# Kernel optimization log

Hardware: AMD Instinct MI355X
Metric: run time of the kernel (lower is better)

The kernel has to match this reference:

```python
import jax, jax.numpy as jnp
import numpy as np

SEQ, IN, H = 64, 100000, 50


def setup_inputs() -> dict:
    key = jax.random.key(0)
    k0, k1, k2, k3, k4 = jax.random.split(key, 5)
    x = jax.random.normal(k0, (SEQ, 1, IN), dtype=jnp.float32) * 0.02
    Wi = jax.random.normal(k1, (IN, 4 * H), dtype=jnp.float32) * 0.01
    bi = jax.random.normal(k2, (4 * H,), dtype=jnp.float32) * 0.01
    Wh = jax.random.normal(k3, (H, 4 * H), dtype=jnp.float32) * 0.1
    bh = jax.random.normal(k4, (4 * H,), dtype=jnp.float32) * 0.01
    return {"x": x, "Wi": Wi, "bi": bi, "Wh": Wh, "bh": bh}


def reference(x, Wi, bi, Wh, bh):
    # x: [seq, batch=1, input_size] -- each row is a flattened ParameterList.
    # Precompute the input projection for all steps at once (one big GEMM),
    # same math as per-step input_weights(input) since it has no recurrence.
    gates_in = jnp.einsum('sbi,ig->sbg', x, Wi) + bi + bh  # [seq, 1, 4H]

    def step(carry, g_in):
        hx, cx = carry
        gates = g_in + hx @ Wh  # [1, 4H]
        i, f, g, o = jnp.split(gates, 4, axis=1)
        i = jax.nn.sigmoid(i)
        f = jax.nn.sigmoid(f)
        g = jnp.tanh(g)
        o = jax.nn.sigmoid(o)
        cy = f * cx + i * g
        hy = o * jnp.tanh(cy)
        return (hy, cy), None

    h0 = jnp.zeros((1, H), dtype=x.dtype)
    c0 = jnp.zeros((1, H), dtype=x.dtype)
    (h_final, _), _ = jax.lax.scan(step, (h0, c0), gates_in)
    # torch.squeeze(out_hidden): (1, H) -> (H,)
    return jnp.squeeze(h_final)
```

## Files before the change

### kernel.cpp

```cpp
#include <hip/hip_runtime.h>
#include <hip/hip_bf16.h>


#define K_DIM 100000
#define NG 200
#define NS 64
#define TK 32
#define NBLK 512
#define KSTRIDE (NBLK * TK)
#define CELLS (NS * NG)
#define XS_STRIDE 68

__global__ __launch_bounds__(512, 4) void k1_gemm_partial(
    const float* __restrict__ x, const float* __restrict__ Wi,
    float* __restrict__ partial)
{
    __shared__ float4 ws4[TK * 50];
    __shared__ float  xs[TK * XS_STRIDE];

    const int tid  = threadIdx.x;
    const int lane = tid & 63;
    const int wave = tid >> 6;
    const int s0   = wave * 8;

    const int sx = tid >> 3;
    const int kq = (tid & 7) << 2;
    const float4* wi4 = (const float4*)Wi;

    float4 acc4[8];
#pragma unroll
    for (int j = 0; j < 8; ++j) acc4[j] = make_float4(0.f, 0.f, 0.f, 0.f);

    int kt = blockIdx.x * TK;

    float4 w0, w1, w2, w3 = make_float4(0.f, 0.f, 0.f, 0.f), xr;
    {
        const float4* wt = wi4 + (size_t)kt * 50;
        w0 = wt[tid];
        w1 = wt[tid + 512];
        w2 = wt[tid + 1024];
        if (tid < 64) w3 = wt[tid + 1536];
        xr = *(const float4*)(x + (size_t)sx * K_DIM + kt + kq);
    }

    for (; kt < K_DIM; kt += KSTRIDE) {
        __syncthreads();
        ws4[tid]        = w0;
        ws4[tid + 512]  = w1;
        ws4[tid + 1024] = w2;
        if (tid < 64) ws4[tid + 1536] = w3;
        xs[(kq + 0) * XS_STRIDE + sx] = xr.x;
        xs[(kq + 1) * XS_STRIDE + sx] = xr.y;
        xs[(kq + 2) * XS_STRIDE + sx] = xr.z;
        xs[(kq + 3) * XS_STRIDE + sx] = xr.w;
        __syncthreads();

        int ktn = kt + KSTRIDE;
        if (ktn < K_DIM) {
            const float4* wt = wi4 + (size_t)ktn * 50;
            w0 = wt[tid];
            w1 = wt[tid + 512];
            w2 = wt[tid + 1024];
            if (tid < 64) w3 = wt[tid + 1536];
            xr = *(const float4*)(x + (size_t)sx * K_DIM + ktn + kq);
        }

        if (lane < 50) {
#pragma unroll 4
            for (int k = 0; k < TK; ++k) {
                float4 wv = ws4[k * 50 + lane];
                const float4* xrow = (const float4*)(xs + k * XS_STRIDE + s0);
                float4 xa = xrow[0];
                float4 xb = xrow[1];
                acc4[0].x = fmaf(wv.x, xa.x, acc4[0].x);
                acc4[0].y = fmaf(wv.y, xa.x, acc4[0].y);
                acc4[0].z = fmaf(wv.z, xa.x, acc4[0].z);
                acc4[0].w = fmaf(wv.w, xa.x, acc4[0].w);
                acc4[1].x = fmaf(wv.x, xa.y, acc4[1].x);
                acc4[1].y = fmaf(wv.y, xa.y, acc4[1].y);
                acc4[1].z = fmaf(wv.z, xa.y, acc4[1].z);
                acc4[1].w = fmaf(wv.w, xa.y, acc4[1].w);
                acc4[2].x = fmaf(wv.x, xa.z, acc4[2].x);
                acc4[2].y = fmaf(wv.y, xa.z, acc4[2].y);
                acc4[2].z = fmaf(wv.z, xa.z, acc4[2].z);
                acc4[2].w = fmaf(wv.w, xa.z, acc4[2].w);
                acc4[3].x = fmaf(wv.x, xa.w, acc4[3].x);
                acc4[3].y = fmaf(wv.y, xa.w, acc4[3].y);
                acc4[3].z = fmaf(wv.z, xa.w, acc4[3].z);
                acc4[3].w = fmaf(wv.w, xa.w, acc4[3].w);
                acc4[4].x = fmaf(wv.x, xb.x, acc4[4].x);
                acc4[4].y = fmaf(wv.y, xb.x, acc4[4].y);
                acc4[4].z = fmaf(wv.z, xb.x, acc4[4].z);
                acc4[4].w = fmaf(wv.w, xb.x, acc4[4].w);
                acc4[5].x = fmaf(wv.x, xb.y, acc4[5].x);
                acc4[5].y = fmaf(wv.y, xb.y, acc4[5].y);
                acc4[5].z = fmaf(wv.z, xb.y, acc4[5].z);
                acc4[5].w = fmaf(wv.w, xb.y, acc4[5].w);
                acc4[6].x = fmaf(wv.x, xb.z, acc4[6].x);
                acc4[6].y = fmaf(wv.y, xb.z, acc4[6].y);
                acc4[6].z = fmaf(wv.z, xb.z, acc4[6].z);
                acc4[6].w = fmaf(wv.w, xb.z, acc4[6].w);
                acc4[7].x = fmaf(wv.x, xb.w, acc4[7].x);
                acc4[7].y = fmaf(wv.y, xb.w, acc4[7].y);
                acc4[7].z = fmaf(wv.z, xb.w, acc4[7].z);
                acc4[7].w = fmaf(wv.w, xb.w, acc4[7].w);
            }
        }
    }

    if (lane < 50) {
        float4* pout = (float4*)(partial + (size_t)blockIdx.x * CELLS) + lane;
#pragma unroll
        for (int si = 0; si < 8; ++si)
            pout[(s0 + si) * 50] = acc4[si];
    }
}

__global__ __launch_bounds__(256) void k2_reduce(
    const float* __restrict__ partial, const float* __restrict__ bi,
    const float* __restrict__ bh, float* __restrict__ gates)
{
    __shared__ float red[256];
    const int tid   = threadIdx.x;
    const int lane  = tid & 63;
    const int slice = tid >> 6;
    const int cell  = blockIdx.x * 64 + lane;

    float sum = 0.f;
#pragma unroll 8
    for (int b = slice * 128; b < (slice + 1) * 128; ++b)
        sum += partial[(size_t)b * CELLS + cell];
    red[tid] = sum;
    __syncthreads();
    if (slice == 0) {
        float tot = red[lane] + red[64 + lane] + red[128 + lane] + red[192 + lane];
        int g = cell % NG;
        gates[cell] = tot + bi[g] + bh[g];
    }
}

__global__ __launch_bounds__(256) void k3_lstm(
    const float* __restrict__ gates, const float* __restrict__ Wh,
    float* __restrict__ out)
{
    __shared__ float gz[CELLS];
    __shared__ float h_lds[64];
    __shared__ float act_lds[NG];
    const int g = threadIdx.x;

    for (int i = g; i < CELLS; i += 256) gz[i] = gates[i];

    float wh[50];
    if (g < NG) {
#pragma unroll
        for (int j = 0; j < 50; ++j) wh[j] = Wh[j * NG + g];
    }
    if (g < 64) h_lds[g] = 0.f;
    float c = 0.f, h = 0.f;
    const bool is_cell_gate = (g >= 100 && g < 150);
    __syncthreads();

    for (int s = 0; s < 64; ++s) {
        if (g < NG) {
            float a0 = gz[s * NG + g];
            float a1 = 0.f;
#pragma unroll
            for (int jj = 0; jj < 50; jj += 2) {
                float2 h2 = *(const float2*)(h_lds + jj);
                a0 = fmaf(h2.x, wh[jj],     a0);
                a1 = fmaf(h2.y, wh[jj + 1], a1);
            }
            float z = a0 + a1;
            float e   = __expf(-z);
            float sig = 1.f / (1.f + e);
            float e2  = e * e;
            float th  = (1.f - e2) / (1.f + e2);
            act_lds[g] = is_cell_gate ? th : sig;
        }
        __syncthreads();
        if (g < 50) {
            float iv = act_lds[g];
            float fv = act_lds[50 + g];
            float gv = act_lds[100 + g];
            float ov = act_lds[150 + g];
            c = fmaf(fv, c, iv * gv);
            float e2c = __expf(-2.f * c);
            h = ov * (1.f - e2c) / (1.f + e2c);
            h_lds[g] = h;
        }
        __syncthreads();
    }
    if (g < 50) out[g] = h;
}

extern "C" void kernel_launch(void* const* d_in, const int* in_sizes, int n_in,
                              void* d_out, int out_size, void* d_ws, size_t ws_size,
                              hipStream_t stream)
{
    const float* x  = (const float*)d_in[0];
    const float* Wi = (const float*)d_in[1];
    const float* bi = (const float*)d_in[2];
    const float* Wh = (const float*)d_in[3];
    const float* bh = (const float*)d_in[4];
    float* out = (float*)d_out;

    float* partial = (float*)d_ws;
    float* gates   = partial + (size_t)NBLK * CELLS;

    k1_gemm_partial<<<NBLK, 512, 0, stream>>>(x, Wi, partial);
    k2_reduce<<<CELLS / 64, 256, 0, stream>>>(partial, bi, bh, gates);
    k3_lstm<<<1, 256, 0, stream>>>(gates, Wh, out);
}
```

Baseline: 205.2 us.

## Load x via wave-uniform global reads instead of LDS staging; widen reduce

The GEMM kernel no longer stages x in shared memory. Each wave reads its 8 sequence rows straight from global memory using wave-uniform addresses (readfirstlane), which lets the compiler use scalar loads, and it prefetches the next 4-column chunk in registers. The lane<50 guard is dropped and the LDS weight buffer is padded so the extra lanes read in bounds; their results are never stored. The reduce kernel moves to 512 threads with 8 slices to shorten each thread's serial sum. The aim is to cut LDS traffic and bank pressure in the inner loop, at the cost of more global/scalar load latency and some wasted lanes.

```diff
diff --git a/kernel.cpp b/kernel.cpp
--- a/kernel.cpp
+++ b/kernel.cpp
@@ -9,38 +9,32 @@
 #define NBLK 512
 #define KSTRIDE (NBLK * TK)
 #define CELLS (NS * NG)
-#define XS_STRIDE 68
 
 __global__ __launch_bounds__(512, 4) void k1_gemm_partial(
     const float* __restrict__ x, const float* __restrict__ Wi,
     float* __restrict__ partial)
 {
-    __shared__ float4 ws4[TK * 50];
-    __shared__ float  xs[TK * XS_STRIDE];
+    __shared__ float4 ws4[TK * 50 + 16];
 
     const int tid  = threadIdx.x;
     const int lane = tid & 63;
     const int wave = tid >> 6;
-    const int s0   = wave * 8;
-
-    const int sx = tid >> 3;
-    const int kq = (tid & 7) << 2;
-    const float4* wi4 = (const float4*)Wi;
+    const int s0u  = __builtin_amdgcn_readfirstlane(wave * 8);
 
     float4 acc4[8];
 #pragma unroll
     for (int j = 0; j < 8; ++j) acc4[j] = make_float4(0.f, 0.f, 0.f, 0.f);
 
     int kt = blockIdx.x * TK;
+    const float4* wi4 = (const float4*)Wi;
 
-    float4 w0, w1, w2, w3 = make_float4(0.f, 0.f, 0.f, 0.f), xr;
+    float4 w0, w1, w2, w3 = make_float4(0.f, 0.f, 0.f, 0.f);
     {
         const float4* wt = wi4 + (size_t)kt * 50;
         w0 = wt[tid];
         w1 = wt[tid + 512];
         w2 = wt[tid + 1024];
         if (tid < 64) w3 = wt[tid + 1536];
-        xr = *(const float4*)(x + (size_t)sx * K_DIM + kt + kq);
     }
 
     for (; kt < K_DIM; kt += KSTRIDE) {
@@ -49,10 +43,6 @@
         ws4[tid + 512]  = w1;
         ws4[tid + 1024] = w2;
         if (tid < 64) ws4[tid + 1536] = w3;
-        xs[(kq + 0) * XS_STRIDE + sx] = xr.x;
-        xs[(kq + 1) * XS_STRIDE + sx] = xr.y;
-        xs[(kq + 2) * XS_STRIDE + sx] = xr.z;
-        xs[(kq + 3) * XS_STRIDE + sx] = xr.w;
         __syncthreads();
 
         int ktn = kt + KSTRIDE;
@@ -62,48 +52,37 @@
             w1 = wt[tid + 512];
             w2 = wt[tid + 1024];
             if (tid < 64) w3 = wt[tid + 1536];
-            xr = *(const float4*)(x + (size_t)sx * K_DIM + ktn + kq);
         }
 
-        if (lane < 50) {
-#pragma unroll 4
-            for (int k = 0; k < TK; ++k) {
-                float4 wv = ws4[k * 50 + lane];
-                const float4* xrow = (const float4*)(xs + k * XS_STRIDE + s0);
-                float4 xa = xrow[0];
-                float4 xb = xrow[1];
-                acc4[0].x = fmaf(wv.x, xa.x, acc4[0].x);
-                acc4[0].y = fmaf(wv.y, xa.x, acc4[0].y);
-                acc4[0].z = fmaf(wv.z, xa.x, acc4[0].z);
-                acc4[0].w = fmaf(wv.w, xa.x, acc4[0].w);
-                acc4[1].x = fmaf(wv.x, xa.y, acc4[1].x);
-                acc4[1].y = fmaf(wv.y, xa.y, acc4[1].y);
-                acc4[1].z = fmaf(wv.z, xa.y, acc4[1].z);
-                acc4[1].w = fmaf(wv.w, xa.y, acc4[1].w);
-                acc4[2].x = fmaf(wv.x, xa.z, acc4[2].x);
-                acc4[2].y = fmaf(wv.y, xa.z, acc4[2].y);
-                acc4[2].z = fmaf(wv.z, xa.z, acc4[2].z);
-                acc4[2].w = fmaf(wv.w, xa.z, acc4[2].w);
-                acc4[3].x = fmaf(wv.x, xa.w, acc4[3].x);
-                acc4[3].y = fmaf(wv.y, xa.w, acc4[3].y);
-                acc4[3].z = fmaf(wv.z, xa.w, acc4[3].z);
-                acc4[3].w = fmaf(wv.w, xa.w, acc4[3].w);
-                acc4[4].x = fmaf(wv.x, xb.x, acc4[4].x);
-                acc4[4].y = fmaf(wv.y, xb.x, acc4[4].y);
-                acc4[4].z = fmaf(wv.z, xb.x, acc4[4].z);
-                acc4[4].w = fmaf(wv.w, xb.x, acc4[4].w);
-                acc4[5].x = fmaf(wv.x, xb.y, acc4[5].x);
-                acc4[5].y = fmaf(wv.y, xb.y, acc4[5].y);
-                acc4[5].z = fmaf(wv.z, xb.y, acc4[5].z);
-                acc4[5].w = fmaf(wv.w, xb.y, acc4[5].w);
-                acc4[6].x = fmaf(wv.x, xb.z, acc4[6].x);
-                acc4[6].y = fmaf(wv.y, xb.z, acc4[6].y);
-                acc4[6].z = fmaf(wv.z, xb.z, acc4[6].z);
-                acc4[6].w = fmaf(wv.w, xb.z, acc4[6].w);
-                acc4[7].x = fmaf(wv.x, xb.w, acc4[7].x);
-                acc4[7].y = fmaf(wv.y, xb.w, acc4[7].y);
-                acc4[7].z = fmaf(wv.z, xb.w, acc4[7].z);
-                acc4[7].w = fmaf(wv.w, xb.w, acc4[7].w);
+        const float* xt = x + (size_t)s0u * K_DIM + kt;
+        float4 xc[8], xn[8];
+#pragma unroll
+        for (int i = 0; i < 8; ++i)
+            xc[i] = *(const float4*)(xt + (size_t)i * K_DIM);
+
+#pragma unroll
+        for (int k4 = 0; k4 < TK / 4; ++k4) {
+            if (k4 + 1 < TK / 4) {
+#pragma unroll
+                for (int i = 0; i < 8; ++i)
+                    xn[i] = *(const float4*)(xt + (size_t)i * K_DIM + (k4 + 1) * 4);
+            }
+#pragma unroll
+            for (int kk = 0; kk < 4; ++kk) {
+                float4 wv = ws4[(k4 * 4 + kk) * 50 + lane];
+#pragma unroll
+                for (int i = 0; i < 8; ++i) {
+                    float xv = (kk == 0) ? xc[i].x : (kk == 1) ? xc[i].y
+                             : (kk == 2) ? xc[i].z : xc[i].w;
+                    acc4[i].x = fmaf(wv.x, xv, acc4[i].x);
+                    acc4[i].y = fmaf(wv.y, xv, acc4[i].y);
+                    acc4[i].z = fmaf(wv.z, xv, acc4[i].z);
+                    acc4[i].w = fmaf(wv.w, xv, acc4[i].w);
+                }
+            }
+            if (k4 + 1 < TK / 4) {
+#pragma unroll
+                for (int i = 0; i < 8; ++i) xc[i] = xn[i];
             }
         }
     }
@@ -112,15 +91,15 @@
         float4* pout = (float4*)(partial + (size_t)blockIdx.x * CELLS) + lane;
 #pragma unroll
         for (int si = 0; si < 8; ++si)
-            pout[(s0 + si) * 50] = acc4[si];
+            pout[(s0u + si) * 50] = acc4[si];
     }
 }
 
-__global__ __launch_bounds__(256) void k2_reduce(
+__global__ __launch_bounds__(512) void k2_reduce(
     const float* __restrict__ partial, const float* __restrict__ bi,
     const float* __restrict__ bh, float* __restrict__ gates)
 {
-    __shared__ float red[256];
+    __shared__ float red[512];
     const int tid   = threadIdx.x;
     const int lane  = tid & 63;
     const int slice = tid >> 6;
@@ -128,12 +107,14 @@
 
     float sum = 0.f;
 #pragma unroll 8
-    for (int b = slice * 128; b < (slice + 1) * 128; ++b)
+    for (int b = slice * 64; b < (slice + 1) * 64; ++b)
         sum += partial[(size_t)b * CELLS + cell];
     red[tid] = sum;
     __syncthreads();
     if (slice == 0) {
-        float tot = red[lane] + red[64 + lane] + red[128 + lane] + red[192 + lane];
+        float tot = red[lane];
+#pragma unroll
+        for (int p = 1; p < 8; ++p) tot += red[p * 64 + lane];
         int g = cell % NG;
         gates[cell] = tot + bi[g] + bh[g];
     }
@@ -208,6 +189,6 @@
     float* gates   = partial + (size_t)NBLK * CELLS;
 
     k1_gemm_partial<<<NBLK, 512, 0, stream>>>(x, Wi, partial);
-    k2_reduce<<<CELLS / 64, 256, 0, stream>>>(partial, bi, bh, gates);
+    k2_reduce<<<CELLS / 64, 512, 0, stream>>>(partial, bi, bh, gates);
     k3_lstm<<<1, 256, 0, stream>>>(gates, Wh, out);
 }
```

After: 208.6 us. No clear change (+1.7%).
